# Optimization experiments

Measured on AMD Instinct MI355X. Metric: run time of the kernel, lower is better.

The kernel has to match this reference:

```python
import jax, jax.numpy as jnp
import numpy as np

THETA_ALPHA = 160.0  # spatial bandwidth of bilateral kernel
THETA_BETA = 3.0     # color bandwidth of bilateral kernel
THETA_GAMMA = 3.0    # spatial bandwidth of spatial kernel
NUM_ITERS = 5        # mean-field iterations


def setup_inputs() -> dict:
    key = jax.random.key(0)
    ks = jax.random.split(key, 5)
    B, H, W, C = 1, 80, 80, 21
    unaries = jax.random.normal(ks[0], (B, H, W, C), dtype=jnp.float32)
    image = jax.random.uniform(ks[1], (B, H, W, 3), dtype=jnp.float32) * 255.0
    spatial_w = jax.random.normal(ks[2], (C, C), dtype=jnp.float32) * 0.1 + jnp.eye(C)
    bilateral_w = jax.random.normal(ks[3], (C, C), dtype=jnp.float32) * 0.1 + jnp.eye(C)
    compat = jax.random.normal(ks[4], (C, C), dtype=jnp.float32) * 0.1 - jnp.eye(C)
    return {"unaries": unaries, "image": image, "spatial_w": spatial_w,
            "bilateral_w": bilateral_w, "compat": compat}


def _gauss_kernel(feat):
    # feat: [N, F] -> dense Gaussian affinity exp(-0.5*||f_i - f_j||^2), [N, N]
    sq = jnp.sum(feat * feat, axis=-1)
    d2 = sq[:, None] + sq[None, :] - 2.0 * (feat @ feat.T)
    return jnp.exp(-0.5 * jnp.maximum(d2, 0.0))


def reference(unaries, image, spatial_w, bilateral_w, compat):
    B, H, W, C = unaries.shape
    N = H * W
    yy, xx = jnp.meshgrid(jnp.arange(H, dtype=jnp.float32),
                          jnp.arange(W, dtype=jnp.float32), indexing="ij")
    pos = jnp.stack([yy, xx], axis=-1).reshape(N, 2)          # [N, 2]
    rgb = image.reshape(N, 3)
    feat_s = pos / THETA_GAMMA                                 # spatial kernel features
    feat_b = jnp.concatenate([pos / THETA_ALPHA, rgb / THETA_BETA], axis=-1)
    Ks = _gauss_kernel(feat_s)                                 # [N, N]
    Kb = _gauss_kernel(feat_b)                                 # [N, N]
    norm_s = jnp.sum(Ks, axis=-1, keepdims=True)               # splat-of-ones normalization
    norm_b = jnp.sum(Kb, axis=-1, keepdims=True)
    u = unaries.reshape(N, C)
    q = u
    for _ in range(NUM_ITERS):
        p = jax.nn.softmax(q, axis=-1)                         # [N, C]
        msg = (Ks @ p) / norm_s @ spatial_w.T + (Kb @ p) / norm_b @ bilateral_w.T
        q = u - msg @ compat.T                                 # compatibility transform
    return q.reshape(B, H, W, C)
```

## Files before the change

### kernel.cpp

```cpp
#include <hip/hip_runtime.h>


#define HH 80
#define WW 80
#define NPIX 6400
#define CC 21
#define PP 24
#define NITER 5
#define NCAP 64
#define SCAP 48
#define SADGATE 23u
#define RAD 14

typedef short short8 __attribute__((ext_vector_type(8)));
union H8 { short8 v; unsigned short u[8]; };

__device__ __forceinline__ float bf2f(unsigned short h) {
    return __uint_as_float(((unsigned)h) << 16);
}
__device__ __forceinline__ unsigned short f2bf(float f) {
    unsigned u = __float_as_uint(f);
    return (unsigned short)((u + 0x7fffu + ((u >> 16) & 1u)) >> 16);
}

__global__ void __launch_bounds__(1024) nbr_kernel(const float* __restrict__ image,
        const float* __restrict__ unaries,
        const float* __restrict__ sw, const float* __restrict__ bw,
        const float* __restrict__ ct,
        int* __restrict__ nbr_j, float* __restrict__ nbr_k, int* __restrict__ nbr_cnt,
        float* __restrict__ norm_b, float* __restrict__ Stab,
        float* __restrict__ csw_g, float* __restrict__ cbw_g,
        unsigned short* __restrict__ p0) {
    __shared__ unsigned int cimg[NPIX];
    int tid = threadIdx.x;
    int bid = blockIdx.x;
    for (int px = tid; px < NPIX; px += 1024) {
        float r = image[px * 3 + 0], g = image[px * 3 + 1], b = image[px * 3 + 2];
        unsigned ur = (unsigned)(r + 0.5f), ug = (unsigned)(g + 0.5f), ub = (unsigned)(b + 0.5f);
        cimg[px] = ur | (ug << 8) | (ub << 16);
    }
    if (bid == 0) {
        if (tid < HH) {
            float s = 0.f;
            float t = (float)tid;
            for (int tp = 0; tp < HH; ++tp) {
                float d = t - (float)tp;
                s += __expf(-d * d * (1.0f / 18.0f));
            }
            Stab[tid] = s;
        }
        for (int idx = tid; idx < 2 * CC * CC; idx += 1024) {
            int m = idx % (CC * CC);
            int c = m / CC, k = m % CC;
            const float* wmat = (idx < CC * CC) ? sw : bw;
            float s = 0.f;
            for (int mm = 0; mm < CC; ++mm) s += ct[c * CC + mm] * wmat[mm * CC + k];
            if (idx < CC * CC) csw_g[m] = s; else cbw_g[m] = s;
        }
    }
    __syncthreads();
    int lane = tid & 63;
    int i = bid * 16 + (tid >> 6);
    unsigned ci = cimg[i];
    float eir = image[i * 3 + 0], eig = image[i * 3 + 1], eib = image[i * 3 + 2];
    float yi = (float)(i / WW), xi = (float)(i % WW);
    int base = 0;
    float ksum = 0.f;
    for (int j0 = 0; j0 < NPIX; j0 += 64) {
        int j = j0 + lane;
        unsigned cj = cimg[j];
#if __has_builtin(__builtin_amdgcn_sad_u8)
        unsigned sad = __builtin_amdgcn_sad_u8(ci, cj, 0u);
#else
        int dr = (int)(ci & 255u) - (int)(cj & 255u);
        int dg = (int)((ci >> 8) & 255u) - (int)((cj >> 8) & 255u);
        int db = (int)((ci >> 16) & 255u) - (int)((cj >> 16) & 255u);
        unsigned sad = (unsigned)(abs(dr) + abs(dg) + abs(db));
#endif
        bool pass = (sad <= SADGATE);
        unsigned long long mask = __ballot(pass);
        if (pass) {
            int slot = base + __popcll(mask & ((1ull << lane) - 1ull));
            if (slot < NCAP) {
                float er = eir - image[j * 3 + 0];
                float eg = eig - image[j * 3 + 1];
                float eb = eib - image[j * 3 + 2];
                float dy = (yi - (float)(j / WW)) * (1.0f / 160.0f);
                float dx = (xi - (float)(j % WW)) * (1.0f / 160.0f);
                float d2 = (er * er + eg * eg + eb * eb) * (1.0f / 9.0f) + dy * dy + dx * dx;
                float kk = __expf(-0.5f * d2);
                nbr_j[i * NCAP + slot] = j;
                nbr_k[i * NCAP + slot] = kk;
                ksum += kk;
            }
        }
        base += (int)__popcll(mask);
    }
    for (int off = 32; off > 0; off >>= 1) ksum += __shfl_down(ksum, off, 64);
    if (lane == 0) {
        nbr_cnt[i] = (base < NCAP) ? base : NCAP;
        norm_b[i] = ksum;
    }
    float v = (lane < CC) ? unaries[i * CC + lane] : -1e30f;
    float m = v;
    for (int off = 16; off > 0; off >>= 1) m = fmaxf(m, __shfl_down(m, off, 32));
    m = __shfl(m, 0, 32);
    float e = (lane < CC) ? __expf(v - m) : 0.f;
    float s = e;
    for (int off = 16; off > 0; off >>= 1) s += __shfl_down(s, off, 32);
    s = __shfl(s, 0, 32);
    if (lane < PP) p0[i * PP + lane] = (lane < CC) ? f2bf(e / s) : (unsigned short)0;
}

__global__ void __launch_bounds__(256) iter_kernel(const float* __restrict__ unaries,
        const unsigned short* __restrict__ pc,
        const int* __restrict__ nbr_j, const float* __restrict__ nbr_k,
        const int* __restrict__ nbr_cnt, const float* __restrict__ norm_b,
        const float* __restrict__ Stab,
        const float* __restrict__ csw_g, const float* __restrict__ cbw_g,
        unsigned short* __restrict__ pn, float* __restrict__ out, int last) {
    __shared__ float lcsw[CC * CC], lcbw[CC * CC];
    __shared__ float gl[16];
    __shared__ float cy[2 * 38 * PP];
    __shared__ float asb[20 * PP];
    __shared__ float abb[2][20 * PP];
    __shared__ float ebuf[20 * PP];
    __shared__ int   njl[20][SCAP];
    __shared__ float nkl[20][SCAP];
    __shared__ int   cnt_l[20];
    __shared__ float inv_ns[20];

    int tid = threadIdx.x;
    int y0 = (blockIdx.x >> 3) * 2;
    int x0 = (blockIdx.x & 7) * 10;
    int xs = (x0 - RAD > 0) ? x0 - RAD : 0;
    int xe = (x0 + 10 + RAD < WW) ? x0 + 10 + RAD : WW;
    int extw = xe - xs;
    const short8* pc8 = (const short8*)pc;

    for (int idx = tid; idx < 2 * CC * CC; idx += 256) {
        if (idx < CC * CC) lcsw[idx] = csw_g[idx];
        else lcbw[idx - CC * CC] = cbw_g[idx - CC * CC];
    }
    if (tid < 16) { float d = (float)tid; gl[tid] = __expf(-d * d * (1.0f / 18.0f)); }
    if (tid >= 32 && tid < 52) {
        int px = tid - 32;
        int yl = px / 10, xl = px % 10;
        int i = (y0 + yl) * WW + x0 + xl;
        int cnt = nbr_cnt[i]; if (cnt > SCAP) cnt = SCAP;
        cnt_l[px] = cnt;
        inv_ns[px] = 1.0f / (Stab[y0 + yl] * Stab[x0 + xl]);
    }
    for (int idx = tid; idx < 20 * SCAP; idx += 256) {
        int px = idx / SCAP, sl = idx % SCAP;
        int yl = px / 10, xl = px % 10;
        int i = (y0 + yl) * WW + x0 + xl;
        int cnt = nbr_cnt[i]; if (cnt > SCAP) cnt = SCAP;
        if (sl < cnt) {
            njl[px][sl] = nbr_j[i * NCAP + sl];
            nkl[px][sl] = nbr_k[i * NCAP + sl] / norm_b[i];
        }
    }
    __syncthreads();

    int climit = extw * 3;
    for (int idx = tid; idx < climit + 120; idx += 256) {
        if (idx < climit) {
            int xl = idx / 3, grp = idx % 3;
            int x = xs + xl;
            int ys_ = (y0 - RAD > 0) ? y0 - RAD : 0;
            int ye_ = (y0 + 1 + RAD < HH - 1) ? y0 + 1 + RAD : HH - 1;
            float a0[8] = {0,0,0,0,0,0,0,0}, a1[8] = {0,0,0,0,0,0,0,0};
            for (int yp = ys_; yp <= ye_; ++yp) {
                H8 h; h.v = pc8[(yp * WW + x) * 3 + grp];
                int d0 = y0 - yp; if (d0 < 0) d0 = -d0;
                int d1 = y0 + 1 - yp; if (d1 < 0) d1 = -d1;
                float g0 = gl[d0], g1 = gl[d1];
                #pragma unroll
                for (int e = 0; e < 8; ++e) {
                    float f = bf2f(h.u[e]);
                    a0[e] += g0 * f; a1[e] += g1 * f;
                }
            }
            #pragma unroll
            for (int e = 0; e < 8; ++e) {
                cy[(0 * 38 + xl) * PP + grp * 8 + e] = a0[e];
                cy[(1 * 38 + xl) * PP + grp * 8 + e] = a1[e];
            }
        } else {
            int g = idx - climit;
            int px = g / 6, r = g % 6;
            int grp = r >> 1, h = r & 1;
            int cnt = cnt_l[px];
            float acc[8] = {0,0,0,0,0,0,0,0};
            for (int n = h; n < cnt; n += 2) {
                int j = njl[px][n];
                float kk = nkl[px][n];
                H8 hv; hv.v = pc8[j * 3 + grp];
                #pragma unroll
                for (int e = 0; e < 8; ++e) acc[e] += kk * bf2f(hv.u[e]);
            }
            #pragma unroll
            for (int e = 0; e < 8; ++e) abb[h][px * PP + grp * 8 + e] = acc[e];
        }
    }
    __syncthreads();

    for (int idx = tid; idx < 420; idx += 256) {
        int px = idx / CC, c = idx % CC;
        int yl = px / 10, xl = px % 10;
        int x = x0 + xl;
        int q0 = (x - RAD > 0) ? x - RAD : 0;
        int q1 = (x + RAD < WW - 1) ? x + RAD : WW - 1;
        float s = 0.f;
        for (int xp = q0; xp <= q1; ++xp) {
            int d = x - xp; if (d < 0) d = -d;
            s += gl[d] * cy[(yl * 38 + (xp - xs)) * PP + c];
        }
        asb[px * PP + c] = s * inv_ns[px];
    }
    __syncthreads();

    for (int idx = tid; idx < 420; idx += 256) {
        int px = idx / CC, c = idx % CC;
        int yl = px / 10, xl = px % 10;
        int i = (y0 + yl) * WW + x0 + xl;
        float m = 0.f;
        #pragma unroll
        for (int k = 0; k < CC; ++k)
            m += lcsw[c * CC + k] * asb[px * PP + k]
               + lcbw[c * CC + k] * (abb[0][px * PP + k] + abb[1][px * PP + k]);
        float qv = unaries[i * CC + c] - m;
        if (last) out[i * CC + c] = qv;
        else ebuf[px * PP + c] = __expf(qv);
    }
    if (!last) {
        __syncthreads();
        for (int idx = tid; idx < 480; idx += 256) {
            int px = idx / PP, c = idx % PP;
            int yl = px / 10, xl = px % 10;
            int i = (y0 + yl) * WW + x0 + xl;
            if (c < CC) {
                float s = 0.f;
                #pragma unroll
                for (int cc = 0; cc < CC; ++cc) s += ebuf[px * PP + cc];
                pn[i * PP + c] = f2bf(ebuf[px * PP + c] / s);
            } else {
                pn[i * PP + c] = 0;
            }
        }
    }
}

extern "C" void kernel_launch(void* const* d_in, const int* in_sizes, int n_in,
                              void* d_out, int out_size, void* d_ws, size_t ws_size,
                              hipStream_t stream) {
    const float* unaries = (const float*)d_in[0];
    const float* image   = (const float*)d_in[1];
    const float* sw      = (const float*)d_in[2];
    const float* bw      = (const float*)d_in[3];
    const float* ct      = (const float*)d_in[4];
    float* out = (float*)d_out;

    char* ws = (char*)d_ws;
    size_t off = 0;
    auto alloc = [&](size_t bytes) -> char* {
        char* p = ws + off;
        off += (bytes + 255) & ~(size_t)255;
        return p;
    };
    int*   nbr_j   = (int*)alloc((size_t)NPIX * NCAP * 4);
    float* nbr_k   = (float*)alloc((size_t)NPIX * NCAP * 4);
    int*   nbr_cnt = (int*)alloc((size_t)NPIX * 4);
    float* norm_b  = (float*)alloc((size_t)NPIX * 4);
    unsigned short* pA = (unsigned short*)alloc((size_t)NPIX * PP * 2);
    unsigned short* pB = (unsigned short*)alloc((size_t)NPIX * PP * 2);
    float* Stab    = (float*)alloc(HH * 4);
    float* csw_g   = (float*)alloc(CC * CC * 4);
    float* cbw_g   = (float*)alloc(CC * CC * 4);
    (void)ws_size;

    nbr_kernel<<<400, 1024, 0, stream>>>(image, unaries, sw, bw, ct,
                                         nbr_j, nbr_k, nbr_cnt, norm_b, Stab,
                                         csw_g, cbw_g, pA);
    unsigned short* pc = pA;
    unsigned short* pn = pB;
    for (int t = 0; t < NITER; ++t) {
        iter_kernel<<<320, 256, 0, stream>>>(unaries, pc, nbr_j, nbr_k, nbr_cnt,
                                             norm_b, Stab, csw_g, cbw_g, pn, out,
                                             (t == NITER - 1) ? 1 : 0);
        unsigned short* tsw = pc; pc = pn; pn = tsw;
    }
}
```

Before: 160.5 us.

## Shrink iteration tile to one row and map threads per pixel-channel

Each iteration block now covers a 1x10 pixel strip instead of 2x10, launching 640 blocks of 320 threads instead of 320 blocks of 256. Each 32-lane group owns one pixel, with one lane per channel. The bilateral neighbour gather moves into the horizontal spatial-pass stage as per-channel scalar loads. The softmax normalisation uses a warp shuffle instead of an extra shared buffer and barrier. This is meant to raise parallelism and remove a synchronisation stage, at the cost of losing the two-row reuse of the vertical pass and doing a longer serial gather loop per thread.

After: 145.7 us. 9.2% less time.

```diff
diff --git a/kernel.cpp b/kernel.cpp
--- a/kernel.cpp
+++ b/kernel.cpp
@@ -112,7 +112,7 @@
     if (lane < PP) p0[i * PP + lane] = (lane < CC) ? f2bf(e / s) : (unsigned short)0;
 }
 
-__global__ void __launch_bounds__(256) iter_kernel(const float* __restrict__ unaries,
+__global__ void __launch_bounds__(320) iter_kernel(const float* __restrict__ unaries,
         const unsigned short* __restrict__ pc,
         const int* __restrict__ nbr_j, const float* __restrict__ nbr_k,
         const int* __restrict__ nbr_cnt, const float* __restrict__ norm_b,
@@ -121,40 +121,36 @@
         unsigned short* __restrict__ pn, float* __restrict__ out, int last) {
     __shared__ float lcsw[CC * CC], lcbw[CC * CC];
     __shared__ float gl[16];
-    __shared__ float cy[2 * 38 * PP];
-    __shared__ float asb[20 * PP];
-    __shared__ float abb[2][20 * PP];
-    __shared__ float ebuf[20 * PP];
-    __shared__ int   njl[20][SCAP];
-    __shared__ float nkl[20][SCAP];
-    __shared__ int   cnt_l[20];
-    __shared__ float inv_ns[20];
+    __shared__ float cy[38 * PP];
+    __shared__ float asb[10 * 25], abb[10 * 25];
+    __shared__ int   njl[10][SCAP];
+    __shared__ float nkl[10][SCAP];
+    __shared__ int   cnt_l[10];
+    __shared__ float inv_ns[10];
 
     int tid = threadIdx.x;
-    int y0 = (blockIdx.x >> 3) * 2;
+    int y = blockIdx.x >> 3;
     int x0 = (blockIdx.x & 7) * 10;
     int xs = (x0 - RAD > 0) ? x0 - RAD : 0;
     int xe = (x0 + 10 + RAD < WW) ? x0 + 10 + RAD : WW;
     int extw = xe - xs;
     const short8* pc8 = (const short8*)pc;
 
-    for (int idx = tid; idx < 2 * CC * CC; idx += 256) {
+    for (int idx = tid; idx < 2 * CC * CC; idx += 320) {
         if (idx < CC * CC) lcsw[idx] = csw_g[idx];
         else lcbw[idx - CC * CC] = cbw_g[idx - CC * CC];
     }
     if (tid < 16) { float d = (float)tid; gl[tid] = __expf(-d * d * (1.0f / 18.0f)); }
-    if (tid >= 32 && tid < 52) {
+    if (tid >= 32 && tid < 42) {
         int px = tid - 32;
-        int yl = px / 10, xl = px % 10;
-        int i = (y0 + yl) * WW + x0 + xl;
+        int i = y * WW + x0 + px;
         int cnt = nbr_cnt[i]; if (cnt > SCAP) cnt = SCAP;
         cnt_l[px] = cnt;
-        inv_ns[px] = 1.0f / (Stab[y0 + yl] * Stab[x0 + xl]);
-    }
-    for (int idx = tid; idx < 20 * SCAP; idx += 256) {
+        inv_ns[px] = 1.0f / (Stab[y] * Stab[x0 + px]);
+    }
+    for (int idx = tid; idx < 10 * SCAP; idx += 320) {
         int px = idx / SCAP, sl = idx % SCAP;
-        int yl = px / 10, xl = px % 10;
-        int i = (y0 + yl) * WW + x0 + xl;
+        int i = y * WW + x0 + px;
         int cnt = nbr_cnt[i]; if (cnt > SCAP) cnt = SCAP;
         if (sl < cnt) {
             njl[px][sl] = nbr_j[i * NCAP + sl];
@@ -163,92 +159,65 @@
     }
     __syncthreads();
 
-    int climit = extw * 3;
-    for (int idx = tid; idx < climit + 120; idx += 256) {
-        if (idx < climit) {
-            int xl = idx / 3, grp = idx % 3;
-            int x = xs + xl;
-            int ys_ = (y0 - RAD > 0) ? y0 - RAD : 0;
-            int ye_ = (y0 + 1 + RAD < HH - 1) ? y0 + 1 + RAD : HH - 1;
-            float a0[8] = {0,0,0,0,0,0,0,0}, a1[8] = {0,0,0,0,0,0,0,0};
-            for (int yp = ys_; yp <= ye_; ++yp) {
-                H8 h; h.v = pc8[(yp * WW + x) * 3 + grp];
-                int d0 = y0 - yp; if (d0 < 0) d0 = -d0;
-                int d1 = y0 + 1 - yp; if (d1 < 0) d1 = -d1;
-                float g0 = gl[d0], g1 = gl[d1];
-                #pragma unroll
-                for (int e = 0; e < 8; ++e) {
-                    float f = bf2f(h.u[e]);
-                    a0[e] += g0 * f; a1[e] += g1 * f;
-                }
-            }
+    if (tid < extw * 3) {
+        int col = tid / 3, grp = tid % 3;
+        int x = xs + col;
+        int ys_ = (y - RAD > 0) ? y - RAD : 0;
+        int ye_ = (y + RAD < HH - 1) ? y + RAD : HH - 1;
+        float a[8] = {0, 0, 0, 0, 0, 0, 0, 0};
+        for (int yp = ys_; yp <= ye_; ++yp) {
+            int d = y - yp; if (d < 0) d = -d;
+            float g = gl[d];
+            H8 h; h.v = pc8[(yp * WW + x) * 3 + grp];
             #pragma unroll
-            for (int e = 0; e < 8; ++e) {
-                cy[(0 * 38 + xl) * PP + grp * 8 + e] = a0[e];
-                cy[(1 * 38 + xl) * PP + grp * 8 + e] = a1[e];
-            }
-        } else {
-            int g = idx - climit;
-            int px = g / 6, r = g % 6;
-            int grp = r >> 1, h = r & 1;
-            int cnt = cnt_l[px];
-            float acc[8] = {0,0,0,0,0,0,0,0};
-            for (int n = h; n < cnt; n += 2) {
-                int j = njl[px][n];
-                float kk = nkl[px][n];
-                H8 hv; hv.v = pc8[j * 3 + grp];
-                #pragma unroll
-                for (int e = 0; e < 8; ++e) acc[e] += kk * bf2f(hv.u[e]);
-            }
-            #pragma unroll
-            for (int e = 0; e < 8; ++e) abb[h][px * PP + grp * 8 + e] = acc[e];
-        }
-    }
-    __syncthreads();
-
-    for (int idx = tid; idx < 420; idx += 256) {
-        int px = idx / CC, c = idx % CC;
-        int yl = px / 10, xl = px % 10;
-        int x = x0 + xl;
+            for (int e = 0; e < 8; ++e) a[e] += g * bf2f(h.u[e]);
+        }
+        #pragma unroll
+        for (int e = 0; e < 8; ++e) cy[col * PP + grp * 8 + e] = a[e];
+    }
+    __syncthreads();
+
+    int px = tid >> 5, c = tid & 31;
+    int x = x0 + px;
+    int i = y * WW + x;
+    if (c < CC) {
         int q0 = (x - RAD > 0) ? x - RAD : 0;
         int q1 = (x + RAD < WW - 1) ? x + RAD : WW - 1;
         float s = 0.f;
         for (int xp = q0; xp <= q1; ++xp) {
             int d = x - xp; if (d < 0) d = -d;
-            s += gl[d] * cy[(yl * 38 + (xp - xs)) * PP + c];
-        }
-        asb[px * PP + c] = s * inv_ns[px];
-    }
-    __syncthreads();
-
-    for (int idx = tid; idx < 420; idx += 256) {
-        int px = idx / CC, c = idx % CC;
-        int yl = px / 10, xl = px % 10;
-        int i = (y0 + yl) * WW + x0 + xl;
-        float m = 0.f;
+            s += gl[d] * cy[(xp - xs) * PP + c];
+        }
+        asb[px * 25 + c] = s * inv_ns[px];
+        int cnt = cnt_l[px];
+        float ab = 0.f;
+        for (int n = 0; n < cnt; ++n)
+            ab += nkl[px][n] * bf2f(pc[njl[px][n] * PP + c]);
+        abb[px * 25 + c] = ab;
+    }
+    __syncthreads();
+
+    if (last) {
+        if (c < CC) {
+            float m = 0.f;
+            #pragma unroll
+            for (int k = 0; k < CC; ++k)
+                m += lcsw[c * CC + k] * asb[px * 25 + k] + lcbw[c * CC + k] * abb[px * 25 + k];
+            out[i * CC + c] = unaries[i * CC + c] - m;
+        }
+    } else {
+        float ev = 0.f;
+        if (c < CC) {
+            float m = 0.f;
+            #pragma unroll
+            for (int k = 0; k < CC; ++k)
+                m += lcsw[c * CC + k] * asb[px * 25 + k] + lcbw[c * CC + k] * abb[px * 25 + k];
+            ev = __expf(unaries[i * CC + c] - m);
+        }
+        float s = ev;
         #pragma unroll
-        for (int k = 0; k < CC; ++k)
-            m += lcsw[c * CC + k] * asb[px * PP + k]
-               + lcbw[c * CC + k] * (abb[0][px * PP + k] + abb[1][px * PP + k]);
-        float qv = unaries[i * CC + c] - m;
-        if (last) out[i * CC + c] = qv;
-        else ebuf[px * PP + c] = __expf(qv);
-    }
-    if (!last) {
-        __syncthreads();
-        for (int idx = tid; idx < 480; idx += 256) {
-            int px = idx / PP, c = idx % PP;
-            int yl = px / 10, xl = px % 10;
-            int i = (y0 + yl) * WW + x0 + xl;
-            if (c < CC) {
-                float s = 0.f;
-                #pragma unroll
-                for (int cc = 0; cc < CC; ++cc) s += ebuf[px * PP + cc];
-                pn[i * PP + c] = f2bf(ebuf[px * PP + c] / s);
-            } else {
-                pn[i * PP + c] = 0;
-            }
-        }
+        for (int off = 16; off > 0; off >>= 1) s += __shfl_xor(s, off, 32);
+        if (c < CC) pn[i * PP + c] = f2bf(ev / s);
     }
 }
 
@@ -286,7 +255,7 @@
     unsigned short* pc = pA;
     unsigned short* pn = pB;
     for (int t = 0; t < NITER; ++t) {
-        iter_kernel<<<320, 256, 0, stream>>>(unaries, pc, nbr_j, nbr_k, nbr_cnt,
+        iter_kernel<<<640, 320, 0, stream>>>(unaries, pc, nbr_j, nbr_k, nbr_cnt,
                                              norm_b, Stab, csw_g, cbw_g, pn, out,
                                              (t == NITER - 1) ? 1 : 0);
         unsigned short* tsw = pc; pc = pn; pn = tsw;
```
